# Optimization experiments

Hardware: AMD Instinct MI355X
Metric: run time of the kernel (lower is better)

## Reference

```python
import jax, jax.numpy as jnp
import numpy as np

D = 2  # NUM_DIM (spatial dimension)


def _mlp(x, params, activate_final=False):
    n = len(params)
    for i, (w, b) in enumerate(params):
        x = x @ w + b
        if i < n - 1 or activate_final:
            x = jnp.tanh(x)
    return x


def _glorot(key, shape):
    fan_in, fan_out = shape[0], shape[-1]
    lim = np.sqrt(6.0 / (fan_in + fan_out)).astype(np.float32)
    return jax.random.uniform(key, shape, jnp.float32, -lim, lim)


def setup_inputs() -> dict:
    key = jax.random.key(0)
    ks = iter(jax.random.split(key, 40))
    B, N, M, K, P, C = 4, 32, 64, 16, 128, 2
    AW, TW, W = 64, 256, 128
    inp = {}
    inp['phase_coords'] = jax.random.normal(next(ks), (B, N, 2 * D), jnp.float32)
    inp['boundary_coords'] = jax.random.normal(next(ks), (B, M, 2 * D), jnp.float32)
    inp['boundary'] = jax.random.uniform(next(ks), (B, M), jnp.float32)
    inp['boundary_weights'] = jax.random.uniform(next(ks), (B, M), jnp.float32)
    inp['position_coords'] = jax.random.normal(next(ks), (B, P, D), jnp.float32)
    inp['sigma'] = jax.random.uniform(next(ks), (B, P, C), jnp.float32)
    inp['velocity_coords'] = jax.random.normal(next(ks), (B, K, D), jnp.float32)
    inp['velocity_weights'] = jax.random.uniform(next(ks), (B, K), jnp.float32)
    inp['scattering_kernel'] = jax.random.uniform(next(ks), (B, N, K), jnp.float32)
    inp['self_scattering_kernel'] = jax.random.uniform(next(ks), (B, K, K), jnp.float32)
    # attention MLP: input 2*D + 2 (coords ++ local frame) -> [64, 64, 1]
    inp['aw0'] = _glorot(next(ks), (2 * D + 2, AW)); inp['ab0'] = jnp.zeros((AW,), jnp.float32)
    inp['aw1'] = _glorot(next(ks), (AW, AW)); inp['ab1'] = jnp.zeros((AW,), jnp.float32)
    inp['aw2'] = _glorot(next(ks), (AW, 1)); inp['ab2'] = jnp.zeros((1,), jnp.float32)
    # transport MLP: input 4*D + C -> [256, 256, 128], activate_final=True
    inp['tw0'] = _glorot(next(ks), (4 * D + C, TW)); inp['tb0'] = jnp.zeros((TW,), jnp.float32)
    inp['tw1'] = _glorot(next(ks), (TW, TW)); inp['tb1'] = jnp.zeros((TW,), jnp.float32)
    inp['tw2'] = _glorot(next(ks), (TW, W)); inp['tb2'] = jnp.zeros((W,), jnp.float32)
    # scattering modules: res_block_depth=2 -> one stacked layer + one final layer
    inp['sw0'] = _glorot(next(ks), (W, W))
    inp['sb0'] = jax.random.uniform(next(ks), (W,), jnp.float32, -0.1, 0.1)
    inp['sw1'] = _glorot(next(ks), (W, W))
    inp['sb1'] = jax.random.uniform(next(ks), (W,), jnp.float32, -0.1, 0.1)
    inp['out_w'] = jax.random.uniform(next(ks), (W,), jnp.float32, -0.1, 0.1)
    return inp


def _forward(phase_coords, boundary_coords, boundary, boundary_weights,
             position_coords, sigma, velocity_coords, velocity_weights,
             scattering_kernel, self_scattering_kernel,
             aw0, ab0, aw1, ab1, aw2, ab2,
             tw0, tb0, tw1, tb1, tw2, tb2,
             sw0, sb0, sw1, sb1, out_w):
    B, N, _ = phase_coords.shape
    M = boundary_coords.shape[1]
    K = velocity_coords.shape[1]
    P = position_coords.shape[1]
    C = sigma.shape[-1]
    K1 = K + 1  # phase velocity v plus the Nv quadrature velocities

    x, v = phase_coords[..., :D], phase_coords[..., D:]          # (B,N,D)
    xp, vp = boundary_coords[..., :D], boundary_coords[..., D:]  # (B,M,D)

    # all velocities at which the transport MLP is evaluated: (B,N,K1,D)
    vall = jnp.concatenate(
        [v[:, :, None, :],
         jnp.broadcast_to(velocity_coords[:, None, :, :], (B, N, K, D))], axis=2)

    # ---- CoefficientNet (geometry-masked MLP attention over coeff positions) ----
    coords = jnp.concatenate(
        [jnp.broadcast_to(x[:, :, None, :], (B, N, K1, D)), vall], axis=-1)  # (B,N,K1,2D)
    ang_g = vall / jnp.sqrt(jnp.sum(vall ** 2, axis=-1, keepdims=True) + 1e-16)
    rel = x[:, :, None, :] - position_coords[:, None, :, :]                 # (B,N,P,D)
    rel_dist = jnp.sqrt(jnp.sum(rel ** 2, axis=-1) + 1e-16)                 # (B,N,P)
    pos_local = jnp.einsum('bnpd,bnkd->bnkp', rel, ang_g)                   # (B,N,K1,P)
    ang_local = pos_local / (rel_dist[:, :, None, :] + 1e-8)
    frames = jnp.stack([ang_local, pos_local], axis=-1)                     # (B,N,K1,P,2)
    qk = jnp.concatenate(
        [jnp.broadcast_to(coords[:, :, :, None, :], (B, N, K1, P, 2 * D)), frames], axis=-1)
    logits = _mlp(qk, [(aw0, ab0), (aw1, ab1), (aw2, ab2)])[..., 0]         # (B,N,K1,P)
    attn_w = jax.nn.softmax(jnp.where(pos_local > 0, logits, -1e30), axis=-1)
    coeff = jnp.exp(-jnp.einsum('bnkp,bpc->bnkc', attn_w, sigma))           # (B,N,K1,C)

    # ---- TransportModule: MLP + exp over (B,N,M,K1) ----
    t_in = jnp.concatenate([
        jnp.broadcast_to(x[:, :, None, None, :], (B, N, M, K1, D)),
        jnp.broadcast_to(vall[:, :, None, :, :], (B, N, M, K1, D)),
        jnp.broadcast_to(xp[:, None, :, None, :], (B, N, M, K1, D)),
        jnp.broadcast_to(vp[:, None, :, None, :], (B, N, M, K1, D)),
        jnp.broadcast_to(coeff[:, :, None, :, :], (B, N, M, K1, C)),
    ], axis=-1)
    g = jnp.exp(_mlp(t_in, [(tw0, tb0), (tw1, tb1), (tw2, tb2)], activate_final=True))
    act_v = g[:, :, :, 0, :]       # (B,N,M,W)  at the phase velocity
    act_vstar = g[:, :, :, 1:, :]  # (B,N,M,K,W) at the quadrature velocities

    rw_v = (1.0 - scattering_kernel) * velocity_weights[:, None, :]        # (B,N,K)
    rw_vs = (1.0 - self_scattering_kernel) * velocity_weights[:, None, :]  # (B,K,K)

    def scat_v(act, sw, sb):
        res = jnp.einsum('bnk,bnmkw->bnmw', rw_v, act)
        return jnp.tanh(jnp.einsum('iw,bnmw->bnmi', sw, res) + sb)

    def scat_vs(act, sw, sb):
        res = jnp.einsum('bij,bnmjw->bnmiw', rw_vs, act)
        return jnp.tanh(jnp.einsum('iw,bnmkw->bnmki', sw, res) + sb)

    # layer_stack block (res_block_depth - 1 = 1 layer, shared params within the layer)
    new_v = act_v + scat_v(act_vstar, sw0, sb0)
    act_vstar = act_vstar + scat_vs(act_vstar, sw0, sb0)
    act_v = new_v
    # final scattering module (fresh params) updating act_v with res_weights_v
    green = act_v + scat_v(act_vstar, sw1, sb1)

    gdot = jnp.einsum('bnmw,w->bnm', green, out_w)
    # quadrature over boundary points
    return jnp.einsum('bnm,bm->bn', gdot, boundary * boundary_weights)


def reference(phase_coords, boundary_coords, boundary, boundary_weights,
              position_coords, sigma, velocity_coords, velocity_weights,
              scattering_kernel, self_scattering_kernel,
              aw0, ab0, aw1, ab1, aw2, ab2,
              tw0, tb0, tw1, tb1, tw2, tb2,
              sw0, sb0, sw1, sb1, out_w):
    return _forward(phase_coords, boundary_coords, boundary, boundary_weights,
                    position_coords, sigma, velocity_coords, velocity_weights,
                    scattering_kernel, self_scattering_kernel,
                    aw0, ab0, aw1, ab1, aw2, ab2,
                    tw0, tb0, tw1, tb1, tw2, tb2,
                    sw0, sb0, sw1, sb1, out_w)
```

## Files before the change

kernel.cpp:

```cpp
#include <hip/hip_runtime.h>
#include <hip/hip_bf16.h>

#define BB 4
#define NN 32
#define MM 64
#define KK 16
#define KK1 17
#define PP 128
#define CC 2

typedef unsigned short ushort_t;
typedef unsigned int uint32;
typedef __attribute__((ext_vector_type(8))) short bhalf8;
typedef __attribute__((ext_vector_type(4))) float floatx4;

__device__ __forceinline__ float fast_tanh(float x) {
    float e = __expf(2.0f * x);
    return 1.0f - 2.0f / (e + 1.0f);
}
__device__ __forceinline__ ushort_t f2b(float f) {
    uint32 u = __float_as_uint(f);
    return (ushort_t)((u + 0x8000u) >> 16);
}
__device__ __forceinline__ float b2f(ushort_t h) {
    return __uint_as_float(((uint32)h) << 16);
}

#define NATTN (BB * NN * KK1)
#define NPREP 768

#define AH0S 72

__global__ __launch_bounds__(256, 4) void prep_attn_kernel(
    const float* __restrict__ phase, const float* __restrict__ posc,
    const float* __restrict__ sigma, const float* __restrict__ velc,
    const float* __restrict__ aw0, const float* __restrict__ aw1,
    const float* __restrict__ ab0, const float* __restrict__ ab1,
    const float* __restrict__ aw2, const float* __restrict__ ab2,
    const float* __restrict__ tw0, ushort_t* __restrict__ u_ws,
    const float* __restrict__ tw1, const float* __restrict__ tw2,
    const float* __restrict__ sw0, const float* __restrict__ sw1,
    const float* __restrict__ tb0, const float* __restrict__ bcoord,
    ushort_t* __restrict__ W1t, ushort_t* __restrict__ W2t,
    ushort_t* __restrict__ S0t, ushort_t* __restrict__ S1t,
    ushort_t* __restrict__ w_ws)
{
    __shared__ __align__(16) ushort_t sAH[128 * AH0S];
    __shared__ float sPL[128];
    __shared__ float sLG[128];
    __shared__ float s_red[16];

    const int blk = blockIdx.x;
    const int tid = threadIdx.x;

    if (blk >= NATTN) {
        int i = (blk - NATTN) * 256 + tid;
        if (i < 65536) {
            int nn = i >> 8, k = i & 255;
            W1t[i] = f2b(tw1[k * 256 + nn]);
        } else if (i < 98304) {
            int j = i - 65536; int nn = j >> 7, k = j & 127;
            (void)nn; (void)k;
            int jj = i - 65536;
            int col = jj >> 8, kk = jj & 255;
            W2t[jj] = f2b(tw2[kk * 128 + col]);
        } else if (i < 114688) {
            S0t[i - 98304] = f2b(sw0[i - 98304]);
        } else if (i < 131072) {
            S1t[i - 114688] = f2b(sw1[i - 114688]);
        } else if (i < 196608) {
            int j = i - 131072;
            int m = j >> 8, c = j & 255;
            float v = bcoord[m * 4 + 0] * tw0[4 * 256 + c]
                    + bcoord[m * 4 + 1] * tw0[5 * 256 + c]
                    + bcoord[m * 4 + 2] * tw0[6 * 256 + c]
                    + bcoord[m * 4 + 3] * tw0[7 * 256 + c]
                    + tb0[c];
            w_ws[j] = f2b(v);
        }
        return;
    }

    const int wave = tid >> 6;
    const int lane = tid & 63;
    const int lrow = lane & 15;
    const int lkg  = lane >> 4;

    const int b = blk / (NN * KK1);
    const int rem = blk % (NN * KK1);
    const int n = rem / KK1;
    const int k = rem % KK1;

    float x0, x1, va0, va1;
    {
        const int p = tid & 127;
        x0 = phase[(b * NN + n) * 4 + 0];
        x1 = phase[(b * NN + n) * 4 + 1];
        if (k == 0) { va0 = phase[(b * NN + n) * 4 + 2]; va1 = phase[(b * NN + n) * 4 + 3]; }
        else { va0 = velc[(b * KK + (k - 1)) * 2 + 0]; va1 = velc[(b * KK + (k - 1)) * 2 + 1]; }
        const float inv = rsqrtf(va0 * va0 + va1 * va1 + 1e-16f);
        const float ag0 = va0 * inv, ag1 = va1 * inv;
        const float px = posc[(b * PP + p) * 2 + 0];
        const float py = posc[(b * PP + p) * 2 + 1];
        const float r0 = x0 - px, r1 = x1 - py;
        const float rd = sqrtf(r0 * r0 + r1 * r1 + 1e-16f);
        const float pl = r0 * ag0 + r1 * ag1;
        const float al = pl / (rd + 1e-8f);
        if (tid < 128) {
            sPL[p] = pl;
            bhalf8 f0;
            f0[0] = (short)f2b(x0); f0[1] = (short)f2b(x1);
            f0[2] = (short)f2b(va0); f0[3] = (short)f2b(va1);
            f0[4] = (short)f2b(al); f0[5] = (short)f2b(pl);
            f0[6] = 0; f0[7] = 0;
            bhalf8 z = {0, 0, 0, 0, 0, 0, 0, 0};
            *(bhalf8*)&sAH[p * 32 + 0] = f0;
            *(bhalf8*)&sAH[p * 32 + 8] = z;
            *(bhalf8*)&sAH[p * 32 + 16] = z;
            *(bhalf8*)&sAH[p * 32 + 24] = z;
        }
    }
    __syncthreads();

    {
        float b0v[4];
        #pragma unroll
        for (int j = 0; j < 4; ++j) b0v[j] = ab0[j * 16 + lrow];
        bhalf8 a[2];
        #pragma unroll
        for (int mtl = 0; mtl < 2; ++mtl)
            a[mtl] = *(const bhalf8*)&sAH[(wave * 32 + mtl * 16 + lrow) * 32 + lkg * 8];
        __syncthreads();
        #pragma unroll
        for (int j = 0; j < 4; ++j) {
            bhalf8 bf;
            #pragma unroll
            for (int i2 = 0; i2 < 8; ++i2) {
                int kk2 = lkg * 8 + i2;
                float v = (kk2 < 6) ? aw0[kk2 * 64 + j * 16 + lrow] : 0.0f;
                bf[i2] = (short)f2b(v);
            }
            #pragma unroll
            for (int mtl = 0; mtl < 2; ++mtl) {
                floatx4 c = {0.f, 0.f, 0.f, 0.f};
                c = __builtin_amdgcn_mfma_f32_16x16x32_bf16(a[mtl], bf, c, 0, 0, 0);
                #pragma unroll
                for (int q = 0; q < 4; ++q) {
                    int row = wave * 32 + mtl * 16 + lkg * 4 + q;
                    sAH[row * AH0S + j * 16 + lrow] = f2b(fast_tanh(c[q] + b0v[j]));
                }
            }
        }
    }
    __syncthreads();

    {
        float b1v[4], w2v[4];
        #pragma unroll
        for (int j = 0; j < 4; ++j) { b1v[j] = ab1[j * 16 + lrow]; w2v[j] = aw2[j * 16 + lrow]; }
        bhalf8 a0[2], a1[2];
        #pragma unroll
        for (int mtl = 0; mtl < 2; ++mtl) {
            int base = (wave * 32 + mtl * 16 + lrow) * AH0S;
            a0[mtl] = *(const bhalf8*)&sAH[base + lkg * 8];
            a1[mtl] = *(const bhalf8*)&sAH[base + 32 + lkg * 8];
        }
        float s[2][4];
        #pragma unroll
        for (int mtl = 0; mtl < 2; ++mtl)
            #pragma unroll
            for (int q = 0; q < 4; ++q) s[mtl][q] = 0.0f;
        #pragma unroll
        for (int j = 0; j < 4; ++j) {
            const int col = j * 16 + lrow;
            bhalf8 bf0, bf1;
            #pragma unroll
            for (int i2 = 0; i2 < 8; ++i2) {
                bf0[i2] = (short)f2b(aw1[(lkg * 8 + i2) * 64 + col]);
                bf1[i2] = (short)f2b(aw1[(32 + lkg * 8 + i2) * 64 + col]);
            }
            #pragma unroll
            for (int mtl = 0; mtl < 2; ++mtl) {
                floatx4 c = {0.f, 0.f, 0.f, 0.f};
                c = __builtin_amdgcn_mfma_f32_16x16x32_bf16(a0[mtl], bf0, c, 0, 0, 0);
                c = __builtin_amdgcn_mfma_f32_16x16x32_bf16(a1[mtl], bf1, c, 0, 0, 0);
                #pragma unroll
                for (int q = 0; q < 4; ++q)
                    s[mtl][q] += fast_tanh(c[q] + b1v[j]) * w2v[j];
            }
        }
        #pragma unroll
        for (int mask = 1; mask <= 8; mask <<= 1)
            #pragma unroll
            for (int mtl = 0; mtl < 2; ++mtl)
                #pragma unroll
                for (int q = 0; q < 4; ++q)
                    s[mtl][q] += __shfl_xor(s[mtl][q], mask, 64);
        if (lrow == 0) {
            #pragma unroll
            for (int mtl = 0; mtl < 2; ++mtl)
                #pragma unroll
                for (int q = 0; q < 4; ++q)
                    sLG[wave * 32 + mtl * 16 + lkg * 4 + q] = s[mtl][q];
        }
    }
    __syncthreads();

    {
        const int p = tid & 127;
        const float ml = (tid < 128 && sPL[p] > 0.0f) ? (sLG[p] + ab2[0]) : -1e30f;
        float mv = ml;
        for (int o = 32; o > 0; o >>= 1) mv = fmaxf(mv, __shfl_xor(mv, o, 64));
        if (lane == 0) s_red[wave] = mv;
        __syncthreads();
        mv = fmaxf(fmaxf(s_red[0], s_red[1]), fmaxf(s_red[2], s_red[3]));

        const float ew = (tid < 128) ? __expf(ml - mv) : 0.0f;
        float sv = ew;
        for (int o = 32; o > 0; o >>= 1) sv += __shfl_xor(sv, o, 64);
        if (lane == 0) s_red[4 + wave] = sv;
        __syncthreads();
        sv = s_red[4] + s_red[5] + s_red[6] + s_red[7];
        const float attn = ew / sv;

        float s0 = (tid < 128) ? attn * sigma[(b * PP + p) * 2 + 0] : 0.0f;
        float s1 = (tid < 128) ? attn * sigma[(b * PP + p) * 2 + 1] : 0.0f;
        for (int o = 32; o > 0; o >>= 1) { s0 += __shfl_xor(s0, o, 64); s1 += __shfl_xor(s1, o, 64); }
        if (lane == 0) { s_red[8 + wave] = s0; s_red[12 + wave] = s1; }
        __syncthreads();

        const float cc0 = __expf(-(s_red[8] + s_red[9] + s_red[10] + s_red[11]));
        const float cc1 = __expf(-(s_red[12] + s_red[13] + s_red[14] + s_red[15]));
        const int ubase = ((b * NN + n) * KK1 + k) * 256;
        const int cc = tid;
        float uv = x0 * tw0[cc] + x1 * tw0[256 + cc]
                 + va0 * tw0[512 + cc] + va1 * tw0[768 + cc]
                 + cc0 * tw0[2048 + cc] + cc1 * tw0[2304 + cc];
        u_ws[ubase + cc] = f2b(uv);
    }
}

#define H0S  264
#define H1S  136
#define GTSs 40
#define AS2S 136
#define V2S  40

#define U_H0A  0
#define U_H1A  8976
#define U_AS   13600
#define U_GTS  0
#define U_GV   5120
#define U_NEWV 5376
#define U_AS2  5632
#define U_V2T  10256
#define U_A2S  15376
#define U_A3   0
#define F_BBW  7944
#define F_RED  7946

__global__ __launch_bounds__(256, 4) void transport_kernel(
    const float* __restrict__ boundary, const float* __restrict__ bweights,
    const float* __restrict__ vweights, const float* __restrict__ scat,
    const float* __restrict__ selfscat,
    const ushort_t* __restrict__ W1t, const ushort_t* __restrict__ W2t,
    const ushort_t* __restrict__ S0t, const ushort_t* __restrict__ S1t,
    const float* __restrict__ tb1, const float* __restrict__ tb2,
    const float* __restrict__ sb0, const float* __restrict__ sb1,
    const float* __restrict__ outw,
    const ushort_t* __restrict__ u_ws, const ushort_t* __restrict__ w_ws,
    float* __restrict__ out)
{
    __shared__ __align__(16) ushort_t smem[15900];
    float* smf = (float*)smem;

    const int tid = threadIdx.x;
    const int wave = tid >> 6;
    const int lane = tid & 63;
    const int lrow = lane & 15;
    const int lkg  = lane >> 4;

    const int blk = blockIdx.x;
    const int b  = blk >> 10;
    const int n  = (blk >> 5) & 31;
    const int mg = blk & 31;
    const int m0 = mg * 2;
    const int bn = b * NN + n;

    if (tid < 2)
        smf[F_BBW + tid] = boundary[b * MM + m0 + tid] * bweights[b * MM + m0 + tid];

    for (int idx = tid; idx < 17 * 32; idx += 256) {
        int i = idx >> 5, c = idx & 31;
        float val = 0.0f;
        if (c < 16) {
            float vw = vweights[b * KK + c];
            val = (i < 16) ? (1.0f - selfscat[(b * KK + i) * KK + c]) * vw
                           : (1.0f - scat[bn * KK + c]) * vw;
        }
        smem[U_AS + idx] = f2b(val);
    }

    for (int idx = tid; idx < 34 * 32; idx += 256) {
        int row = idx >> 5, oct = idx & 31;
        int ml = (row >= 17);
        int k = row - ml * 17;
        bhalf8 uu = *(const bhalf8*)(u_ws + (bn * KK1 + k) * 256 + oct * 8);
        bhalf8 ww = *(const bhalf8*)(w_ws + (b * MM + m0 + ml) * 256 + oct * 8);
        bhalf8 hh;
        #pragma unroll
        for (int jj = 0; jj < 8; ++jj)
            hh[jj] = (short)f2b(fast_tanh(b2f((ushort_t)uu[jj]) + b2f((ushort_t)ww[jj])));
        *(bhalf8*)&smem[U_H0A + row * H0S + oct * 8] = hh;
    }
    __syncthreads();

    floatx4 c2[2][3];
    #pragma unroll
    for (int j = 0; j < 2; ++j)
        #pragma unroll
        for (int mt = 0; mt < 3; ++mt) c2[j][mt] = (floatx4){0.f, 0.f, 0.f, 0.f};

    for (int chunk = 0; chunk < 2; ++chunk) {
        if (chunk) __syncthreads();
        floatx4 c1[2][3];
        #pragma unroll
        for (int j = 0; j < 2; ++j)
            #pragma unroll
            for (int mt = 0; mt < 3; ++mt) c1[j][mt] = (floatx4){0.f, 0.f, 0.f, 0.f};
        #pragma unroll
        for (int ks = 0; ks < 8; ++ks) {
            bhalf8 a[3];
            #pragma unroll
            for (int mt = 0; mt < 3; ++mt)
                a[mt] = *(const bhalf8*)&smem[U_H0A + (mt * 16 + lrow) * H0S + ks * 32 + lkg * 8];
            #pragma unroll
            for (int j = 0; j < 2; ++j) {
                int colt = chunk * 8 + wave * 2 + j;
                bhalf8 bf = *(const bhalf8*)(W1t + (colt * 16 + lrow) * 256 + ks * 32 + lkg * 8);
                #pragma unroll
                for (int mt = 0; mt < 3; ++mt)
                    c1[j][mt] = __builtin_amdgcn_mfma_f32_16x16x32_bf16(a[mt], bf, c1[j][mt], 0, 0, 0);
            }
        }
        #pragma unroll
        for (int j = 0; j < 2; ++j) {
            const int lcol = (wave * 2 + j) * 16 + lrow;
            const float bb = tb1[chunk * 128 + lcol];
            #pragma unroll
            for (int mt = 0; mt < 3; ++mt)
                #pragma unroll
                for (int q = 0; q < 4; ++q) {
                    int row = mt * 16 + lkg * 4 + q;
                    if (row < 34)
                        smem[U_H1A + row * H1S + lcol] = f2b(fast_tanh(c1[j][mt][q] + bb));
                }
        }
        __syncthreads();
        #pragma unroll
        for (int ks2 = 0; ks2 < 4; ++ks2) {
            bhalf8 a[3];
            #pragma unroll
            for (int mt = 0; mt < 3; ++mt)
                a[mt] = *(const bhalf8*)&smem[U_H1A + (mt * 16 + lrow) * H1S + ks2 * 32 + lkg * 8];
            #pragma unroll
            for (int j = 0; j < 2; ++j) {
                bhalf8 bf = *(const bhalf8*)(W2t + ((wave * 2 + j) * 16 + lrow) * 256
                                             + chunk * 128 + ks2 * 32 + lkg * 8);
                #pragma unroll
                for (int mt = 0; mt < 3; ++mt)
                    c2[j][mt] = __builtin_amdgcn_mfma_f32_16x16x32_bf16(a[mt], bf, c2[j][mt], 0, 0, 0);
            }
        }
    }

    for (int idx = tid; idx < 1024; idx += 256)
        smem[U_GTS + (idx >> 3) * GTSs + 32 + (idx & 7)] = 0;
    {
        #pragma unroll
        for (int j = 0; j < 2; ++j) {
            const int col = (wave * 2 + j) * 16 + lrow;
            const float bb = tb2[col];
            #pragma unroll
            for (int mt = 0; mt < 3; ++mt)
                #pragma unroll
                for (int q = 0; q < 4; ++q) {
                    int row = mt * 16 + lkg * 4 + q;
                    if (row < 34) {
                        int ml = (row >= 17);
                        int k = row - ml * 17;
                        float g = __expf(fast_tanh(c2[j][mt][q] + bb));
                        if (k == 0) smem[U_GV + ml * 128 + col] = f2b(g);
                        else        smem[U_GTS + col * GTSs + ml * 16 + (k - 1)] = f2b(g);
                    }
                }
        }
    }
    __syncthreads();

    for (int idx = tid; idx < 512; idx += 256) {
        int r = idx >> 5, c = idx & 31;
        smem[U_A2S + idx] = ((c >> 4) == r) ? smem[U_AS + 16 * 32 + (c & 15)] : (ushort_t)0;
    }
    {
        bhalf8 a0 = *(const bhalf8*)&smem[U_AS + lrow * 32 + lkg * 8];
        bhalf8 a1 = *(const bhalf8*)&smem[U_AS + (16 + lrow) * 32 + lkg * 8];
        for (int m = 0; m < 2; ++m) {
            #pragma unroll
            for (int j = 0; j < 2; ++j) {
                int nt = 2 * wave + j;
                bhalf8 bf = *(const bhalf8*)&smem[U_GTS + (nt * 16 + lrow) * GTSs + m * 16 + lkg * 8];
                #pragma unroll
                for (int mt = 0; mt < 2; ++mt) {
                    floatx4 c = {0.f, 0.f, 0.f, 0.f};
                    c = __builtin_amdgcn_mfma_f32_16x16x32_bf16(mt ? a1 : a0, bf, c, 0, 0, 0);
                    #pragma unroll
                    for (int q = 0; q < 4; ++q) {
                        int ic = mt * 16 + lkg * 4 + q;
                        if (ic < 17) {
                            int r2 = (ic == 16) ? m * 17 : m * 17 + 1 + ic;
                            smem[U_AS2 + r2 * AS2S + nt * 16 + lrow] = f2b(c[q]);
                        }
                    }
                }
            }
        }
    }
    __syncthreads();

    {
        floatx4 c3[2][3];
        #pragma unroll
        for (int j = 0; j < 2; ++j)
            #pragma unroll
            for (int mt = 0; mt < 3; ++mt) c3[j][mt] = (floatx4){0.f, 0.f, 0.f, 0.f};
        #pragma unroll
        for (int ks = 0; ks < 4; ++ks) {
            bhalf8 a[3];
            #pragma unroll
            for (int mt = 0; mt < 3; ++mt)
                a[mt] = *(const bhalf8*)&smem[U_AS2 + (mt * 16 + lrow) * AS2S + ks * 32 + lkg * 8];
            #pragma unroll
            for (int j = 0; j < 2; ++j) {
                bhalf8 bf = *(const bhalf8*)(S0t + ((2 * wave + j) * 16 + lrow) * 128 + ks * 32 + lkg * 8);
                #pragma unroll
                for (int mt = 0; mt < 3; ++mt)
                    c3[j][mt] = __builtin_amdgcn_mfma_f32_16x16x32_bf16(a[mt], bf, c3[j][mt], 0, 0, 0);
            }
        }
        #pragma unroll
        for (int j = 0; j < 2; ++j) {
            const int col = (2 * wave + j) * 16 + lrow;
            const float bb = sb0[col];
            #pragma unroll
            for (int mt = 0; mt < 3; ++mt)
                #pragma unroll
                for (int q = 0; q < 4; ++q) {
                    int r2 = mt * 16 + lkg * 4 + q;
                    if (r2 < 34) {
                        int m = (r2 >= 17);
                        int i2 = r2 - m * 17;
                        float val = fast_tanh(c3[j][mt][q] + bb);
                        if (i2 == 0) {
                            smem[U_NEWV + m * 128 + col] =
                                f2b(b2f(smem[U_GV + m * 128 + col]) + val);
                        } else {
                            int j2 = i2 - 1;
                            smem[U_V2T + col * V2S + m * 16 + j2] =
                                f2b(b2f(smem[U_GTS + col * GTSs + m * 16 + j2]) + val);
                        }
                    }
                }
        }
    }
    __syncthreads();

    {
        bhalf8 a = *(const bhalf8*)&smem[U_A2S + lrow * 32 + lkg * 8];
        #pragma unroll
        for (int j = 0; j < 2; ++j) {
            int nt = 2 * wave + j;
            bhalf8 bf = *(const bhalf8*)&smem[U_V2T + (nt * 16 + lrow) * V2S + lkg * 8];
            floatx4 c = {0.f, 0.f, 0.f, 0.f};
            c = __builtin_amdgcn_mfma_f32_16x16x32_bf16(a, bf, c, 0, 0, 0);
            #pragma unroll
            for (int q = 0; q < 4; ++q) {
                int r = lkg * 4 + q;
                smem[U_A3 + r * AS2S + nt * 16 + lrow] = f2b(c[q]);
            }
        }
    }
    __syncthreads();

    float acc = 0.0f;
    {
        bhalf8 a[4];
        #pragma unroll
        for (int ks = 0; ks < 4; ++ks)
            a[ks] = *(const bhalf8*)&smem[U_A3 + lrow * AS2S + ks * 32 + lkg * 8];
        #pragma unroll
        for (int j = 0; j < 2; ++j) {
            int nt = 2 * wave + j;
            float s1v = sb1[nt * 16 + lrow];
            float owv = outw[nt * 16 + lrow];
            floatx4 c = {0.f, 0.f, 0.f, 0.f};
            #pragma unroll
            for (int ks = 0; ks < 4; ++ks) {
                bhalf8 bf = *(const bhalf8*)(S1t + (nt * 16 + lrow) * 128 + ks * 32 + lkg * 8);
                c = __builtin_amdgcn_mfma_f32_16x16x32_bf16(a[ks], bf, c, 0, 0, 0);
            }
            #pragma unroll
            for (int q = 0; q < 4; ++q) {
                int r = lkg * 4 + q;
                if (r < 2) {
                    int col = nt * 16 + lrow;
                    float green = b2f(smem[U_NEWV + r * 128 + col]) + fast_tanh(c[q] + s1v);
                    acc += green * owv * smf[F_BBW + r];
                }
            }
        }
    }
    for (int o = 32; o > 0; o >>= 1) acc += __shfl_xor(acc, o, 64);
    if (lane == 0) smf[F_RED + wave] = acc;
    __syncthreads();
    if (tid == 0) {
        float tot = smf[F_RED + 0] + smf[F_RED + 1] + smf[F_RED + 2] + smf[F_RED + 3];
        atomicAdd(&out[bn], tot);
    }
}

extern "C" void kernel_launch(void* const* d_in, const int* in_sizes, int n_in,
                              void* d_out, int out_size, void* d_ws, size_t ws_size,
                              hipStream_t stream) {
    const float* phase    = (const float*)d_in[0];
    const float* bcoord   = (const float*)d_in[1];
    const float* boundary = (const float*)d_in[2];
    const float* bweights = (const float*)d_in[3];
    const float* posc     = (const float*)d_in[4];
    const float* sigma    = (const float*)d_in[5];
    const float* velc     = (const float*)d_in[6];
    const float* vweights = (const float*)d_in[7];
    const float* scat     = (const float*)d_in[8];
    const float* selfscat = (const float*)d_in[9];
    const float* aw0 = (const float*)d_in[10];
    const float* ab0 = (const float*)d_in[11];
    const float* aw1 = (const float*)d_in[12];
    const float* ab1 = (const float*)d_in[13];
    const float* aw2 = (const float*)d_in[14];
    const float* ab2 = (const float*)d_in[15];
    const float* tw0 = (const float*)d_in[16];
    const float* tb0 = (const float*)d_in[17];
    const float* tw1 = (const float*)d_in[18];
    const float* tb1 = (const float*)d_in[19];
    const float* tw2 = (const float*)d_in[20];
    const float* tb2 = (const float*)d_in[21];
    const float* sw0 = (const float*)d_in[22];
    const float* sb0 = (const float*)d_in[23];
    const float* sw1 = (const float*)d_in[24];
    const float* sb1 = (const float*)d_in[25];
    const float* outw = (const float*)d_in[26];

    float* out = (float*)d_out;
    char* ws = (char*)d_ws;
    ushort_t* W1t  = (ushort_t*)(ws + 0);
    ushort_t* W2t  = (ushort_t*)(ws + 131072);
    ushort_t* S0t  = (ushort_t*)(ws + 196608);
    ushort_t* S1t  = (ushort_t*)(ws + 229376);
    ushort_t* u_ws = (ushort_t*)(ws + 262144);
    ushort_t* w_ws = (ushort_t*)(ws + 1376256);

    hipMemsetAsync(d_out, 0, (size_t)out_size * sizeof(float), stream);

    prep_attn_kernel<<<NATTN + NPREP, 256, 0, stream>>>(
        phase, posc, sigma, velc, aw0, aw1, ab0, ab1, aw2, ab2, tw0, u_ws,
        tw1, tw2, sw0, sw1, tb0, bcoord, W1t, W2t, S0t, S1t, w_ws);

    transport_kernel<<<BB * NN * 32, 256, 0, stream>>>(
        boundary, bweights, vweights, scat, selfscat,
        W1t, W2t, S0t, S1t, tb1, tb2, sb0, sb1, outw, u_ws, w_ws, out);
}
```

Baseline: 287.9 us.

## Double transport block to 512 threads, one 16-column tile per wave

Transport kernel blocks grow from 4 to 8 waves. Each wave now owns a single 16-column output tile instead of two, and the reduction sums eight per-wave partials. This halves per-wave accumulator registers and MFMA work to raise parallelism and occupancy, at the cost of more threads contending for barriers and shared memory per block. The A-fragment LDS reads are now duplicated across twice as many waves.

Result: no change. 289.7 us (+0.6%).

```diff
diff --git a/kernel.cpp b/kernel.cpp
--- a/kernel.cpp
+++ b/kernel.cpp
@@ -59,8 +59,6 @@
             int nn = i >> 8, k = i & 255;
             W1t[i] = f2b(tw1[k * 256 + nn]);
         } else if (i < 98304) {
-            int j = i - 65536; int nn = j >> 7, k = j & 127;
-            (void)nn; (void)k;
             int jj = i - 65536;
             int col = jj >> 8, kk = jj & 255;
             W2t[jj] = f2b(tw2[kk * 128 + col]);
@@ -259,7 +257,7 @@
 #define F_BBW  7944
 #define F_RED  7946
 
-__global__ __launch_bounds__(256, 4) void transport_kernel(
+__global__ __launch_bounds__(512, 8) void transport_kernel(
     const float* __restrict__ boundary, const float* __restrict__ bweights,
     const float* __restrict__ vweights, const float* __restrict__ scat,
     const float* __restrict__ selfscat,
@@ -271,7 +269,7 @@
     const ushort_t* __restrict__ u_ws, const ushort_t* __restrict__ w_ws,
     float* __restrict__ out)
 {
-    __shared__ __align__(16) ushort_t smem[15900];
+    __shared__ __align__(16) ushort_t smem[15908];
     float* smf = (float*)smem;
 
     const int tid = threadIdx.x;
@@ -290,7 +288,7 @@
     if (tid < 2)
         smf[F_BBW + tid] = boundary[b * MM + m0 + tid] * bweights[b * MM + m0 + tid];
 
-    for (int idx = tid; idx < 17 * 32; idx += 256) {
+    for (int idx = tid; idx < 17 * 32; idx += 512) {
         int i = idx >> 5, c = idx & 31;
         float val = 0.0f;
         if (c < 16) {
@@ -301,7 +299,7 @@
         smem[U_AS + idx] = f2b(val);
     }
 
-    for (int idx = tid; idx < 34 * 32; idx += 256) {
+    for (int idx = tid; idx < 34 * 32; idx += 512) {
         int row = idx >> 5, oct = idx & 31;
         int ml = (row >= 17);
         int k = row - ml * 17;
@@ -315,37 +313,29 @@
     }
     __syncthreads();
 
-    floatx4 c2[2][3];
+    floatx4 c2[3];
     #pragma unroll
-    for (int j = 0; j < 2; ++j)
-        #pragma unroll
-        for (int mt = 0; mt < 3; ++mt) c2[j][mt] = (floatx4){0.f, 0.f, 0.f, 0.f};
+    for (int mt = 0; mt < 3; ++mt) c2[mt] = (floatx4){0.f, 0.f, 0.f, 0.f};
 
     for (int chunk = 0; chunk < 2; ++chunk) {
         if (chunk) __syncthreads();
-        floatx4 c1[2][3];
-        #pragma unroll
-        for (int j = 0; j < 2; ++j)
-            #pragma unroll
-            for (int mt = 0; mt < 3; ++mt) c1[j][mt] = (floatx4){0.f, 0.f, 0.f, 0.f};
+        floatx4 c1[3];
+        #pragma unroll
+        for (int mt = 0; mt < 3; ++mt) c1[mt] = (floatx4){0.f, 0.f, 0.f, 0.f};
         #pragma unroll
         for (int ks = 0; ks < 8; ++ks) {
             bhalf8 a[3];
             #pragma unroll
             for (int mt = 0; mt < 3; ++mt)
                 a[mt] = *(const bhalf8*)&smem[U_H0A + (mt * 16 + lrow) * H0S + ks * 32 + lkg * 8];
-            #pragma unroll
-            for (int j = 0; j < 2; ++j) {
-                int colt = chunk * 8 + wave * 2 + j;
-                bhalf8 bf = *(const bhalf8*)(W1t + (colt * 16 + lrow) * 256 + ks * 32 + lkg * 8);
-                #pragma unroll
-                for (int mt = 0; mt < 3; ++mt)
-                    c1[j][mt] = __builtin_amdgcn_mfma_f32_16x16x32_bf16(a[mt], bf, c1[j][mt], 0, 0, 0);
-            }
-        }
-        #pragma unroll
-        for (int j = 0; j < 2; ++j) {
-            const int lcol = (wave * 2 + j) * 16 + lrow;
+            int colt = chunk * 8 + wave;
+            bhalf8 bf = *(const bhalf8*)(W1t + (colt * 16 + lrow) * 256 + ks * 32 + lkg * 8);
+            #pragma unroll
+            for (int mt = 0; mt < 3; ++mt)
+                c1[mt] = __builtin_amdgcn_mfma_f32_16x16x32_bf16(a[mt], bf, c1[mt], 0, 0, 0);
+        }
+        {
+            const int lcol = wave * 16 + lrow;
             const float bb = tb1[chunk * 128 + lcol];
             #pragma unroll
             for (int mt = 0; mt < 3; ++mt)
@@ -353,7 +343,7 @@
                 for (int q = 0; q < 4; ++q) {
                     int row = mt * 16 + lkg * 4 + q;
                     if (row < 34)
-                        smem[U_H1A + row * H1S + lcol] = f2b(fast_tanh(c1[j][mt][q] + bb));
+                        smem[U_H1A + row * H1S + lcol] = f2b(fast_tanh(c1[mt][q] + bb));
                 }
         }
         __syncthreads();
@@ -363,42 +353,36 @@
             #pragma unroll
             for (int mt = 0; mt < 3; ++mt)
                 a[mt] = *(const bhalf8*)&smem[U_H1A + (mt * 16 + lrow) * H1S + ks2 * 32 + lkg * 8];
-            #pragma unroll
-            for (int j = 0; j < 2; ++j) {
-                bhalf8 bf = *(const bhalf8*)(W2t + ((wave * 2 + j) * 16 + lrow) * 256
-                                             + chunk * 128 + ks2 * 32 + lkg * 8);
-                #pragma unroll
-                for (int mt = 0; mt < 3; ++mt)
-                    c2[j][mt] = __builtin_amdgcn_mfma_f32_16x16x32_bf16(a[mt], bf, c2[j][mt], 0, 0, 0);
-            }
-        }
-    }
-
-    for (int idx = tid; idx < 1024; idx += 256)
+            bhalf8 bf = *(const bhalf8*)(W2t + (wave * 16 + lrow) * 256
+                                         + chunk * 128 + ks2 * 32 + lkg * 8);
+            #pragma unroll
+            for (int mt = 0; mt < 3; ++mt)
+                c2[mt] = __builtin_amdgcn_mfma_f32_16x16x32_bf16(a[mt], bf, c2[mt], 0, 0, 0);
+        }
+    }
+
+    for (int idx = tid; idx < 1024; idx += 512)
         smem[U_GTS + (idx >> 3) * GTSs + 32 + (idx & 7)] = 0;
     {
-        #pragma unroll
-        for (int j = 0; j < 2; ++j) {
-            const int col = (wave * 2 + j) * 16 + lrow;
-            const float bb = tb2[col];
-            #pragma unroll
-            for (int mt = 0; mt < 3; ++mt)
-                #pragma unroll
-                for (int q = 0; q < 4; ++q) {
-                    int row = mt * 16 + lkg * 4 + q;
-                    if (row < 34) {
-                        int ml = (row >= 17);
-                        int k = row - ml * 17;
-                        float g = __expf(fast_tanh(c2[j][mt][q] + bb));
-                        if (k == 0) smem[U_GV + ml * 128 + col] = f2b(g);
-                        else        smem[U_GTS + col * GTSs + ml * 16 + (k - 1)] = f2b(g);
-                    }
+        const int col = wave * 16 + lrow;
+        const float bb = tb2[col];
+        #pragma unroll
+        for (int mt = 0; mt < 3; ++mt)
+            #pragma unroll
+            for (int q = 0; q < 4; ++q) {
+                int row = mt * 16 + lkg * 4 + q;
+                if (row < 34) {
+                    int ml = (row >= 17);
+                    int k = row - ml * 17;
+                    float g = __expf(fast_tanh(c2[mt][q] + bb));
+                    if (k == 0) smem[U_GV + ml * 128 + col] = f2b(g);
+                    else        smem[U_GTS + col * GTSs + ml * 16 + (k - 1)] = f2b(g);
                 }
-        }
-    }
-    __syncthreads();
-
-    for (int idx = tid; idx < 512; idx += 256) {
+            }
+    }
+    __syncthreads();
+
+    for (int idx = tid; idx < 512; idx += 512) {
         int r = idx >> 5, c = idx & 31;
         smem[U_A2S + idx] = ((c >> 4) == r) ? smem[U_AS + 16 * 32 + (c & 15)] : (ushort_t)0;
     }
@@ -406,21 +390,17 @@
         bhalf8 a0 = *(const bhalf8*)&smem[U_AS + lrow * 32 + lkg * 8];
         bhalf8 a1 = *(const bhalf8*)&smem[U_AS + (16 + lrow) * 32 + lkg * 8];
         for (int m = 0; m < 2; ++m) {
-            #pragma unroll
-            for (int j = 0; j < 2; ++j) {
-                int nt = 2 * wave + j;
-                bhalf8 bf = *(const bhalf8*)&smem[U_GTS + (nt * 16 + lrow) * GTSs + m * 16 + lkg * 8];
+            bhalf8 bf = *(const bhalf8*)&smem[U_GTS + (wave * 16 + lrow) * GTSs + m * 16 + lkg * 8];
+            #pragma unroll
+            for (int mt = 0; mt < 2; ++mt) {
+                floatx4 c = {0.f, 0.f, 0.f, 0.f};
+                c = __builtin_amdgcn_mfma_f32_16x16x32_bf16(mt ? a1 : a0, bf, c, 0, 0, 0);
                 #pragma unroll
-                for (int mt = 0; mt < 2; ++mt) {
-                    floatx4 c = {0.f, 0.f, 0.f, 0.f};
-                    c = __builtin_amdgcn_mfma_f32_16x16x32_bf16(mt ? a1 : a0, bf, c, 0, 0, 0);
-                    #pragma unroll
-                    for (int q = 0; q < 4; ++q) {
-                        int ic = mt * 16 + lkg * 4 + q;
-                        if (ic < 17) {
-                            int r2 = (ic == 16) ? m * 17 : m * 17 + 1 + ic;
-                            smem[U_AS2 + r2 * AS2S + nt * 16 + lrow] = f2b(c[q]);
-                        }
+                for (int q = 0; q < 4; ++q) {
+                    int ic = mt * 16 + lkg * 4 + q;
+                    if (ic < 17) {
+                        int r2 = (ic == 16) ? m * 17 : m * 17 + 1 + ic;
+                        smem[U_AS2 + r2 * AS2S + wave * 16 + lrow] = f2b(c[q]);
                     }
                 }
             }
@@ -429,65 +409,53 @@
     __syncthreads();
 
     {
-        floatx4 c3[2][3];
-        #pragma unroll
-        for (int j = 0; j < 2; ++j)
-            #pragma unroll
-            for (int mt = 0; mt < 3; ++mt) c3[j][mt] = (floatx4){0.f, 0.f, 0.f, 0.f};
+        floatx4 c3[3];
+        #pragma unroll
+        for (int mt = 0; mt < 3; ++mt) c3[mt] = (floatx4){0.f, 0.f, 0.f, 0.f};
         #pragma unroll
         for (int ks = 0; ks < 4; ++ks) {
             bhalf8 a[3];
             #pragma unroll
             for (int mt = 0; mt < 3; ++mt)
                 a[mt] = *(const bhalf8*)&smem[U_AS2 + (mt * 16 + lrow) * AS2S + ks * 32 + lkg * 8];
-            #pragma unroll
-            for (int j = 0; j < 2; ++j) {
-                bhalf8 bf = *(const bhalf8*)(S0t + ((2 * wave + j) * 16 + lrow) * 128 + ks * 32 + lkg * 8);
-                #pragma unroll
-                for (int mt = 0; mt < 3; ++mt)
-                    c3[j][mt] = __builtin_amdgcn_mfma_f32_16x16x32_bf16(a[mt], bf, c3[j][mt], 0, 0, 0);
-            }
-        }
-        #pragma unroll
-        for (int j = 0; j < 2; ++j) {
-            const int col = (2 * wave + j) * 16 + lrow;
-            const float bb = sb0[col];
-            #pragma unroll
-            for (int mt = 0; mt < 3; ++mt)
-                #pragma unroll
-                for (int q = 0; q < 4; ++q) {
-                    int r2 = mt * 16 + lkg * 4 + q;
-                    if (r2 < 34) {
-                        int m = (r2 >= 17);
-                        int i2 = r2 - m * 17;
-                        float val = fast_tanh(c3[j][mt][q] + bb);
-                        if (i2 == 0) {
-                            smem[U_NEWV + m * 128 + col] =
-                                f2b(b2f(smem[U_GV + m * 128 + col]) + val);
-                        } else {
-                            int j2 = i2 - 1;
-                            smem[U_V2T + col * V2S + m * 16 + j2] =
-                                f2b(b2f(smem[U_GTS + col * GTSs + m * 16 + j2]) + val);
-                        }
+            bhalf8 bf = *(const bhalf8*)(S0t + (wave * 16 + lrow) * 128 + ks * 32 + lkg * 8);
+            #pragma unroll
+            for (int mt = 0; mt < 3; ++mt)
+                c3[mt] = __builtin_amdgcn_mfma_f32_16x16x32_bf16(a[mt], bf, c3[mt], 0, 0, 0);
+        }
+        const int col = wave * 16 + lrow;
+        const float bb = sb0[col];
+        #pragma unroll
+        for (int mt = 0; mt < 3; ++mt)
+            #pragma unroll
+            for (int q = 0; q < 4; ++q) {
+                int r2 = mt * 16 + lkg * 4 + q;
+                if (r2 < 34) {
+                    int m = (r2 >= 17);
+                    int i2 = r2 - m * 17;
+                    float val = fast_tanh(c3[mt][q] + bb);
+                    if (i2 == 0) {
+                        smem[U_NEWV + m * 128 + col] =
+                            f2b(b2f(smem[U_GV + m * 128 + col]) + val);
+                    } else {
+                        int j2 = i2 - 1;
+                        smem[U_V2T + col * V2S + m * 16 + j2] =
+                            f2b(b2f(smem[U_GTS + col * GTSs + m * 16 + j2]) + val);
                     }
                 }
-        }
+            }
     }
     __syncthreads();
 
     {
         bhalf8 a = *(const bhalf8*)&smem[U_A2S + lrow * 32 + lkg * 8];
-        #pragma unroll
-        for (int j = 0; j < 2; ++j) {
-            int nt = 2 * wave + j;
-            bhalf8 bf = *(const bhalf8*)&smem[U_V2T + (nt * 16 + lrow) * V2S + lkg * 8];
-            floatx4 c = {0.f, 0.f, 0.f, 0.f};
-            c = __builtin_amdgcn_mfma_f32_16x16x32_bf16(a, bf, c, 0, 0, 0);
-            #pragma unroll
-            for (int q = 0; q < 4; ++q) {
-                int r = lkg * 4 + q;
-                smem[U_A3 + r * AS2S + nt * 16 + lrow] = f2b(c[q]);
-            }
+        bhalf8 bf = *(const bhalf8*)&smem[U_V2T + (wave * 16 + lrow) * V2S + lkg * 8];
+        floatx4 c = {0.f, 0.f, 0.f, 0.f};
+        c = __builtin_amdgcn_mfma_f32_16x16x32_bf16(a, bf, c, 0, 0, 0);
+        #pragma unroll
+        for (int q = 0; q < 4; ++q) {
+            int r = lkg * 4 + q;
+            smem[U_A3 + r * AS2S + wave * 16 + lrow] = f2b(c[q]);
         }
     }
     __syncthreads();
@@ -498,25 +466,21 @@
         #pragma unroll
         for (int ks = 0; ks < 4; ++ks)
             a[ks] = *(const bhalf8*)&smem[U_A3 + lrow * AS2S + ks * 32 + lkg * 8];
-        #pragma unroll
-        for (int j = 0; j < 2; ++j) {
-            int nt = 2 * wave + j;
-            float s1v = sb1[nt * 16 + lrow];
-            float owv = outw[nt * 16 + lrow];
-            floatx4 c = {0.f, 0.f, 0.f, 0.f};
-            #pragma unroll
-            for (int ks = 0; ks < 4; ++ks) {
-                bhalf8 bf = *(const bhalf8*)(S1t + (nt * 16 + lrow) * 128 + ks * 32 + lkg * 8);
-                c = __builtin_amdgcn_mfma_f32_16x16x32_bf16(a[ks], bf, c, 0, 0, 0);
-            }
-            #pragma unroll
-            for (int q = 0; q < 4; ++q) {
-                int r = lkg * 4 + q;
-                if (r < 2) {
-                    int col = nt * 16 + lrow;
-                    float green = b2f(smem[U_NEWV + r * 128 + col]) + fast_tanh(c[q] + s1v);
-                    acc += green * owv * smf[F_BBW + r];
-                }
+        const int col = wave * 16 + lrow;
+        const float s1v = sb1[col];
+        const float owv = outw[col];
+        floatx4 c = {0.f, 0.f, 0.f, 0.f};
+        #pragma unroll
+        for (int ks = 0; ks < 4; ++ks) {
+            bhalf8 bf = *(const bhalf8*)(S1t + col * 128 + ks * 32 + lkg * 8);
+            c = __builtin_amdgcn_mfma_f32_16x16x32_bf16(a[ks], bf, c, 0, 0, 0);
+        }
+        #pragma unroll
+        for (int q = 0; q < 4; ++q) {
+            int r = lkg * 4 + q;
+            if (r < 2) {
+                float green = b2f(smem[U_NEWV + r * 128 + col]) + fast_tanh(c[q] + s1v);
+                acc += green * owv * smf[F_BBW + r];
             }
         }
     }
@@ -524,7 +488,9 @@
     if (lane == 0) smf[F_RED + wave] = acc;
     __syncthreads();
     if (tid == 0) {
-        float tot = smf[F_RED + 0] + smf[F_RED + 1] + smf[F_RED + 2] + smf[F_RED + 3];
+        float tot = 0.0f;
+        #pragma unroll
+        for (int w = 0; w < 8; ++w) tot += smf[F_RED + w];
         atomicAdd(&out[bn], tot);
     }
 }
@@ -575,7 +541,7 @@
         phase, posc, sigma, velc, aw0, aw1, ab0, ab1, aw2, ab2, tw0, u_ws,
         tw1, tw2, sw0, sw1, tb0, bcoord, W1t, W2t, S0t, S1t, w_ws);
 
-    transport_kernel<<<BB * NN * 32, 256, 0, stream>>>(
+    transport_kernel<<<BB * NN * 32, 512, 0, stream>>>(
         boundary, bweights, vweights, scat, selfscat,
         W1t, W2t, S0t, S1t, tb1, tb2, sb0, sb1, outw, u_ws, w_ws, out);
 }
```
